# Optimization experiments

Measured on AMD Instinct MI355X. Metric: run time of the kernel, lower is better.

Reference implementation:

```python
import jax, jax.numpy as jnp
import numpy as np

GRID = (32, 32)          # 448 // 14
IMG = (448, 448)
SIGMA = 4.0              # anomalib AnomalyMapGenerator default smoothing


def _l2norm(x, axis=-1, eps=1e-12):
    return x / jnp.clip(jnp.linalg.norm(x, axis=axis, keepdims=True), eps, None)


def _gaussian_blur(x, sigma=SIGMA):
    # kornia-style: kernel_size = 2*int(4*sigma+0.5)+1, reflect padding, separable conv
    radius = int(4.0 * sigma + 0.5)
    t = jnp.arange(-radius, radius + 1, dtype=x.dtype)
    k = jnp.exp(-0.5 * (t / sigma) ** 2)
    k = k / k.sum()
    xp = jnp.pad(x, ((0, 0), (0, 0), (radius, radius), (radius, radius)), mode='reflect')
    kh = k.reshape(1, 1, -1, 1)
    kw = k.reshape(1, 1, 1, -1)
    dn = ('NCHW', 'OIHW', 'NCHW')
    y = jax.lax.conv_general_dilated(xp, kh, (1, 1), 'VALID', dimension_numbers=dn)
    return jax.lax.conv_general_dilated(y, kw, (1, 1), 'VALID', dimension_numbers=dn)


def setup_inputs() -> dict:
    key = jax.random.key(0)
    k1, k2 = jax.random.split(key)
    features = jax.random.normal(k1, (8, 1024, 384), dtype=jnp.float32)
    memory_bank = jax.random.normal(k2, (65536, 384), dtype=jnp.float32)
    return {"features": features, "memory_bank": memory_bank}


def reference(features, memory_bank):
    # features: (B, N, D) patch tokens from DINOv2; memory_bank: (M, D)
    b, n, _ = features.shape
    f = _l2norm(features)                 # F.normalize(features, p=2, dim=1) on flattened patches
    mb = _l2norm(memory_bank)             # bank stores normalized embeddings
    sim = jnp.einsum('bnd,md->bnm', f, mb)            # (B, N, M) cosine similarity
    dists = jnp.clip(1.0 - sim, 0.0, 2.0)
    min_dists = dists.min(axis=2)                     # k = num_neighbours = 1 -> row min
    num_top = max(int(n * 0.01), 1)
    top_vals = jax.lax.top_k(min_dists, num_top)[0]
    pred_score = top_vals.mean(axis=1, keepdims=True) # (B, 1)
    amap = min_dists.reshape(b, 1, *GRID)
    amap = jax.image.resize(amap, (b, 1, *IMG), method='bilinear')
    anomaly_map = _gaussian_blur(amap)                # (B, 1, H, W)
    return pred_score, anomaly_map
```

## Files before the change

### kernel.cpp

```cpp
#include <hip/hip_runtime.h>
#include <hip/hip_bf16.h>

#define NROW_F 8192
#define NROW_B 65536
#define KDIM   384
#define BM 256
#define BN 256
#define NSUB 8
#define NGRP (NROW_B / (BN * NSUB))
#define NBM  (NROW_F / BM)
#define NWG  (NBM * NGRP)

#define LDSA 0
#define LDSB 98304
#define LDSS 147456
#define LDSR 98304
#define LDS_TOT 155648

typedef int   i32x4 __attribute__((ext_vector_type(4)));
typedef float f32x4 __attribute__((ext_vector_type(4)));

static __device__ __forceinline__ void stage16(const void* g, void* l) {
  __builtin_amdgcn_global_load_lds(
      (const __attribute__((address_space(1))) unsigned int*)g,
      (__attribute__((address_space(3))) unsigned int*)l, 16, 0, 0);
}

__global__ __launch_bounds__(256) void quantize_rows_kernel(
    const float* __restrict__ in, char* __restrict__ out8,
    float* __restrict__ scales, int nrows) {
  int row  = blockIdx.x * 4 + (threadIdx.x >> 6);
  int lane = threadIdx.x & 63;
  if (row >= nrows) return;
  const float* r = in + (size_t)row * KDIM;
  float v[6];
  float ss = 0.f, mx = 0.f;
#pragma unroll
  for (int i = 0; i < 6; ++i) {
    v[i] = r[lane + i * 64];
    ss += v[i] * v[i];
    mx = fmaxf(mx, fabsf(v[i]));
  }
#pragma unroll
  for (int d = 1; d < 64; d <<= 1) {
    ss += __shfl_xor(ss, d, 64);
    mx = fmaxf(mx, __shfl_xor(mx, d, 64));
  }
  mx = fmaxf(mx, 1e-30f);
  float inv = rsqrtf(fmaxf(ss, 1e-24f));
  float scl = 127.0f / mx;
  if (lane == 0) scales[row] = mx * inv * (1.0f / 127.0f);
  char* o = out8 + (size_t)row * KDIM;
#pragma unroll
  for (int i = 0; i < 6; ++i)
    o[lane + i * 64] = (char)__float2int_rn(v[i] * scl);
}

__global__ __launch_bounds__(1024) void maxsim_kernel(
    const char* __restrict__ F8,
    const char* __restrict__ B8,
    const float* __restrict__ sA,
    const float* __restrict__ sB,
    float* __restrict__ partial) {
  __shared__ __align__(16) char smem[LDS_TOT];

  const int tid  = threadIdx.x;
  const int wv   = tid >> 6;
  const int lane = tid & 63;
  const int l15  = lane & 15;
  const int lhi  = lane >> 4;
  const int wr   = wv >> 2;
  const int wc   = wv & 3;

  const int wg  = (blockIdx.x & 7) * (NWG / 8) + (blockIdx.x >> 3);
  const int bm  = wg & (NBM - 1);
  const int grp = wg >> 5;
  const size_t brow = (size_t)bm * BM;

  const int srow = tid >> 2;
  const int gsw  = (tid & 3) ^ ((tid >> 3) & 3);

  {
    const char* gA = F8 + (size_t)(brow + srow) * KDIM + gsw * 16;
    char* lA = smem + LDSA + wv * 1024;
#pragma unroll
    for (int kt = 0; kt < 6; ++kt)
      stage16(gA + kt * 64, lA + kt * 16384);
  }
  if (wv < 8)
    stage16((const char*)(sB + (size_t)grp * 2048) + tid * 16,
            smem + LDSS + wv * 1024);

  auto stageB = [&](int s2, int koff, int buf) {
    const char* g = B8 + ((size_t)grp * 2048 + s2 * 256 + srow) * KDIM
                    + koff * 64 + gsw * 16;
    stage16(g, smem + LDSB + buf * 16384 + wv * 1024);
  };
  stageB(0, 0, 0);
  stageB(0, 1, 1);

  const int cof = ((l15 >> 1) & 3) << 4;

  auto ldA8 = [&](int k6, int m) -> i32x4 {
    int byte = k6 * 16384 + (wr * 64 + m * 16 + l15) * 64 + ((lhi << 4) ^ cof);
    return *reinterpret_cast<const i32x4*>(smem + LDSA + byte);
  };
  auto ldB8 = [&](int buf, int n) -> i32x4 {
    int byte = buf * 16384 + (wc * 64 + n * 16 + l15) * 64 + ((lhi << 4) ^ cof);
    return *reinterpret_cast<const i32x4*>(smem + LDSB + byte);
  };

  i32x4 acc[4][4];
  f32x4 vm[4];
#pragma unroll
  for (int m = 0; m < 4; ++m) {
    vm[m] = f32x4{-1e30f, -1e30f, -1e30f, -1e30f};
#pragma unroll
    for (int n = 0; n < 4; ++n) acc[m][n] = i32x4{0, 0, 0, 0};
  }

  asm volatile("s_waitcnt vmcnt(1)" ::: "memory");
  __builtin_amdgcn_s_barrier();

  for (int sub = 0; sub < NSUB; ++sub) {
#pragma unroll
    for (int k6 = 0; k6 < 6; ++k6) {
      i32x4 a[4], b[4];
#pragma unroll
      for (int m = 0; m < 4; ++m) a[m] = ldA8(k6, m);
#pragma unroll
      for (int n = 0; n < 4; ++n) b[n] = ldB8(k6 % 3, n);
      asm volatile("s_waitcnt lgkmcnt(0)" ::: "memory");
      __builtin_amdgcn_sched_barrier(0);
      __builtin_amdgcn_s_setprio(1);
#pragma unroll
      for (int n = 0; n < 4; ++n)
#pragma unroll
        for (int m = 0; m < 4; ++m)
          acc[m][n] = __builtin_amdgcn_mfma_i32_16x16x64_i8(
              a[m], b[n], acc[m][n], 0, 0, 0);
      __builtin_amdgcn_s_setprio(0);
      {
        const int s2   = (k6 < 4) ? sub : ((sub + 1) & 7);
        const int koff = (k6 + 2) % 6;
        stageB(s2, koff, (k6 + 2) % 3);
      }
      asm volatile("s_waitcnt vmcnt(1)" ::: "memory");
      __builtin_amdgcn_s_barrier();
    }
    float sb[4];
#pragma unroll
    for (int n = 0; n < 4; ++n)
      sb[n] = *reinterpret_cast<const float*>(
          smem + LDSS + (sub * 256 + wc * 64 + n * 16 + l15) * 4);
#pragma unroll
    for (int m = 0; m < 4; ++m) {
#pragma unroll
      for (int n = 0; n < 4; ++n)
#pragma unroll
        for (int j = 0; j < 4; ++j)
          vm[m][j] = fmaxf(vm[m][j], (float)acc[m][n][j] * sb[n]);
#pragma unroll
      for (int n = 0; n < 4; ++n) acc[m][n] = i32x4{0, 0, 0, 0};
    }
  }

  asm volatile("s_waitcnt vmcnt(0)" ::: "memory");
#pragma unroll
  for (int d = 1; d < 16; d <<= 1)
#pragma unroll
    for (int m = 0; m < 4; ++m)
#pragma unroll
      for (int j = 0; j < 4; ++j)
        vm[m][j] = fmaxf(vm[m][j], __shfl_xor(vm[m][j], d, 64));

  float* red = (float*)(smem + LDSR);
  __syncthreads();
  if (l15 == 0) {
#pragma unroll
    for (int m = 0; m < 4; ++m)
#pragma unroll
      for (int j = 0; j < 4; ++j)
        red[wc * 256 + wr * 64 + m * 16 + lhi * 4 + j] = vm[m][j];
  }
  __syncthreads();
  if (tid < 256) {
    float x = fmaxf(fmaxf(red[tid], red[256 + tid]),
                    fmaxf(red[512 + tid], red[768 + tid]));
    partial[(size_t)grp * NROW_F + brow + tid] = x * sA[brow + tid];
  }
}

__global__ __launch_bounds__(256) void combine_kernel(
    const float* __restrict__ partial, float* __restrict__ md) {
  int r = blockIdx.x * 256 + threadIdx.x;
  if (r >= NROW_F) return;
  float m = -1e30f;
#pragma unroll
  for (int c = 0; c < NGRP; ++c) m = fmaxf(m, partial[(size_t)c * NROW_F + r]);
  float d = 1.0f - m;
  d = fminf(fmaxf(d, 0.0f), 2.0f);
  md[r] = d;
}

__global__ __launch_bounds__(256) void topk_kernel(
    const float* __restrict__ md, float* __restrict__ out) {
  __shared__ float buf[1024];
  __shared__ float svals[256];
  __shared__ int   sidx[256];
  int b = blockIdx.x, tid = threadIdx.x;
  for (int i = tid; i < 1024; i += 256) buf[i] = md[b * 1024 + i];
  __syncthreads();
  float total = 0.f;
  for (int it = 0; it < 10; ++it) {
    float best = -1e30f; int bi = 0;
    for (int i = tid; i < 1024; i += 256)
      if (buf[i] > best) { best = buf[i]; bi = i; }
    svals[tid] = best; sidx[tid] = bi;
    __syncthreads();
    for (int s = 128; s > 0; s >>= 1) {
      if (tid < s && svals[tid + s] > svals[tid]) {
        svals[tid] = svals[tid + s]; sidx[tid] = sidx[tid + s];
      }
      __syncthreads();
    }
    if (tid == 0) { total += svals[0]; buf[sidx[0]] = -1e30f; }
    __syncthreads();
  }
  if (tid == 0) out[b] = total * 0.1f;
}

__global__ __launch_bounds__(256) void build_w_kernel(float* __restrict__ W) {
  int idx = blockIdx.x * 256 + threadIdx.x;
  if (idx >= 448 * 32) return;
  int y = idx >> 5, g = idx & 31;
  float ksum = 0.f, acc = 0.f;
#pragma unroll
  for (int t = -16; t <= 16; ++t) {
    float ft = (float)t * 0.25f;
    float kv = expf(-0.5f * ft * ft);
    ksum += kv;
    int p = y + t;
    p = (p < 0) ? -p : ((p > 447) ? 894 - p : p);
    float src = ((float)p + 0.5f) * (1.0f / 14.0f) - 0.5f;
    float fl = floorf(src);
    int i0 = (int)fl;
    float fr = src - fl;
    int c0 = i0 < 0 ? 0 : (i0 > 31 ? 31 : i0);
    int i1 = i0 + 1;
    int c1 = i1 < 0 ? 0 : (i1 > 31 ? 31 : i1);
    float w = 0.f;
    if (c0 == g) w += 1.0f - fr;
    if (c1 == g) w += fr;
    acc += kv * w;
  }
  W[idx] = acc / ksum;
}

__global__ __launch_bounds__(256) void map_stage1_kernel(
    const float* __restrict__ md, const float* __restrict__ W,
    float* __restrict__ tmp) {
  int idx = blockIdx.x * 256 + threadIdx.x;
  if (idx >= 8 * 448 * 32) return;
  int gx = idx & 31;
  int y  = (idx >> 5) % 448;
  int b  = idx / (448 * 32);
  const float* w = W + y * 32;
  const float* m = md + b * 1024 + gx;
  float s = 0.f;
#pragma unroll
  for (int gy = 0; gy < 32; ++gy) s += w[gy] * m[gy * 32];
  tmp[idx] = s;
}

__global__ __launch_bounds__(256) void map_stage2_kernel(
    const float* __restrict__ tmp, const float* __restrict__ W,
    float* __restrict__ out) {
  int idx = blockIdx.x * 256 + threadIdx.x;
  if (idx >= 8 * 448 * 448) return;
  int x    = idx % 448;
  int ypos = idx / 448;
  const float* w = W + x * 32;
  const float* t = tmp + ypos * 32;
  float s = 0.f;
#pragma unroll
  for (int gx = 0; gx < 32; ++gx) s += w[gx] * t[gx];
  out[idx] = s;
}

extern "C" void kernel_launch(void* const* d_in, const int* in_sizes, int n_in,
                              void* d_out, int out_size, void* d_ws, size_t ws_size,
                              hipStream_t stream) {
  const float* features = (const float*)d_in[0];
  const float* bank     = (const float*)d_in[1];
  float* out = (float*)d_out;

  char* ws = (char*)d_ws;
  char*  mb8     = ws;
  char*  f8      = ws + 25165824;
  float* sB      = (float*)(ws + 28311552);
  float* sA      = (float*)(ws + 28573696);
  float* partial = (float*)(ws + 28606464);
  float* md      = (float*)(ws + 29655040);
  float* W       = (float*)(ws + 29687808);
  float* tmp     = (float*)(ws + 29745152);

  quantize_rows_kernel<<<NROW_B / 4, 256, 0, stream>>>(bank, mb8, sB, NROW_B);
  quantize_rows_kernel<<<NROW_F / 4, 256, 0, stream>>>(features, f8, sA, NROW_F);
  maxsim_kernel<<<NWG, 1024, 0, stream>>>(f8, mb8, sA, sB, partial);
  combine_kernel<<<NROW_F / 256, 256, 0, stream>>>(partial, md);
  topk_kernel<<<8, 256, 0, stream>>>(md, out);
  build_w_kernel<<<(448 * 32 + 255) / 256, 256, 0, stream>>>(W);
  map_stage1_kernel<<<(8 * 448 * 32 + 255) / 256, 256, 0, stream>>>(md, W, tmp);
  map_stage2_kernel<<<(8 * 448 * 448 + 255) / 256, 256, 0, stream>>>(tmp, W, out + 8);
}
```

Measured before the change: 275.3 us.

## Shrink maxsim workgroup to 256 threads with 128-row tiles and double-buffered B

The maxsim GEMM-max kernel now uses 128-row A tiles and 256-thread workgroups, and each wave computes a 64x128 output tile with 32 accumulators. The LDS footprint drops so two workgroups can share a CU. The B staging moves from triple to double buffering, with a barrier placed before the next prefetch, and the bank scales are read from global memory instead of being staged in LDS. This aims for better occupancy and latency hiding, at the cost of higher register pressure and more workgroups re-reading the bank.

```diff
diff --git a/kernel.cpp b/kernel.cpp
--- a/kernel.cpp
+++ b/kernel.cpp
@@ -4,7 +4,7 @@
 #define NROW_F 8192
 #define NROW_B 65536
 #define KDIM   384
-#define BM 256
+#define BM 128
 #define BN 256
 #define NSUB 8
 #define NGRP (NROW_B / (BN * NSUB))
@@ -12,10 +12,9 @@
 #define NWG  (NBM * NGRP)
 
 #define LDSA 0
-#define LDSB 98304
-#define LDSS 147456
-#define LDSR 98304
-#define LDS_TOT 155648
+#define LDSB 49152
+#define LDSR 49152
+#define LDS_TOT 81920
 
 typedef int   i32x4 __attribute__((ext_vector_type(4)));
 typedef float f32x4 __attribute__((ext_vector_type(4)));
@@ -56,7 +55,7 @@
     o[lane + i * 64] = (char)__float2int_rn(v[i] * scl);
 }
 
-__global__ __launch_bounds__(1024) void maxsim_kernel(
+__global__ __launch_bounds__(256, 2) void maxsim_kernel(
     const char* __restrict__ F8,
     const char* __restrict__ B8,
     const float* __restrict__ sA,
@@ -69,12 +68,12 @@
   const int lane = tid & 63;
   const int l15  = lane & 15;
   const int lhi  = lane >> 4;
-  const int wr   = wv >> 2;
-  const int wc   = wv & 3;
+  const int wr   = wv >> 1;
+  const int wc   = wv & 1;
 
   const int wg  = (blockIdx.x & 7) * (NWG / 8) + (blockIdx.x >> 3);
   const int bm  = wg & (NBM - 1);
-  const int grp = wg >> 5;
+  const int grp = wg >> 6;
   const size_t brow = (size_t)bm * BM;
 
   const int srow = tid >> 2;
@@ -84,17 +83,19 @@
     const char* gA = F8 + (size_t)(brow + srow) * KDIM + gsw * 16;
     char* lA = smem + LDSA + wv * 1024;
 #pragma unroll
-    for (int kt = 0; kt < 6; ++kt)
-      stage16(gA + kt * 64, lA + kt * 16384);
-  }
-  if (wv < 8)
-    stage16((const char*)(sB + (size_t)grp * 2048) + tid * 16,
-            smem + LDSS + wv * 1024);
+    for (int kt = 0; kt < 6; ++kt) {
+      stage16(gA + kt * 64,             lA + kt * 8192);
+      stage16(gA + kt * 64 + 64 * KDIM, lA + kt * 8192 + 4096);
+    }
+  }
 
   auto stageB = [&](int s2, int koff, int buf) {
     const char* g = B8 + ((size_t)grp * 2048 + s2 * 256 + srow) * KDIM
                     + koff * 64 + gsw * 16;
-    stage16(g, smem + LDSB + buf * 16384 + wv * 1024);
+    char* l = smem + LDSB + buf * 16384 + wv * 1024;
+#pragma unroll
+    for (int j = 0; j < 4; ++j)
+      stage16(g + (size_t)(j * 64) * KDIM, l + j * 4096);
   };
   stageB(0, 0, 0);
   stageB(0, 1, 1);
@@ -102,70 +103,72 @@
   const int cof = ((l15 >> 1) & 3) << 4;
 
   auto ldA8 = [&](int k6, int m) -> i32x4 {
-    int byte = k6 * 16384 + (wr * 64 + m * 16 + l15) * 64 + ((lhi << 4) ^ cof);
+    int byte = k6 * 8192 + (wr * 64 + m * 16 + l15) * 64 + ((lhi << 4) ^ cof);
     return *reinterpret_cast<const i32x4*>(smem + LDSA + byte);
   };
   auto ldB8 = [&](int buf, int n) -> i32x4 {
-    int byte = buf * 16384 + (wc * 64 + n * 16 + l15) * 64 + ((lhi << 4) ^ cof);
+    int byte = buf * 16384 + (wc * 128 + n * 16 + l15) * 64 + ((lhi << 4) ^ cof);
     return *reinterpret_cast<const i32x4*>(smem + LDSB + byte);
   };
 
-  i32x4 acc[4][4];
+  i32x4 acc[4][8];
   f32x4 vm[4];
 #pragma unroll
   for (int m = 0; m < 4; ++m) {
     vm[m] = f32x4{-1e30f, -1e30f, -1e30f, -1e30f};
 #pragma unroll
-    for (int n = 0; n < 4; ++n) acc[m][n] = i32x4{0, 0, 0, 0};
-  }
-
-  asm volatile("s_waitcnt vmcnt(1)" ::: "memory");
+    for (int n = 0; n < 8; ++n) acc[m][n] = i32x4{0, 0, 0, 0};
+  }
+
+  asm volatile("s_waitcnt vmcnt(4)" ::: "memory");
   __builtin_amdgcn_s_barrier();
 
   for (int sub = 0; sub < NSUB; ++sub) {
 #pragma unroll
     for (int k6 = 0; k6 < 6; ++k6) {
-      i32x4 a[4], b[4];
+      i32x4 a[4], b[8];
 #pragma unroll
       for (int m = 0; m < 4; ++m) a[m] = ldA8(k6, m);
 #pragma unroll
-      for (int n = 0; n < 4; ++n) b[n] = ldB8(k6 % 3, n);
+      for (int n = 0; n < 8; ++n) b[n] = ldB8(k6 & 1, n);
       asm volatile("s_waitcnt lgkmcnt(0)" ::: "memory");
       __builtin_amdgcn_sched_barrier(0);
+      __builtin_amdgcn_s_barrier();
+
+      {
+        const int s2   = (k6 < 4) ? sub : ((sub + 1) & 7);
+        const int koff = (k6 + 2) % 6;
+        stageB(s2, koff, k6 & 1);
+      }
       __builtin_amdgcn_s_setprio(1);
 #pragma unroll
-      for (int n = 0; n < 4; ++n)
+      for (int n = 0; n < 8; ++n)
 #pragma unroll
         for (int m = 0; m < 4; ++m)
           acc[m][n] = __builtin_amdgcn_mfma_i32_16x16x64_i8(
               a[m], b[n], acc[m][n], 0, 0, 0);
       __builtin_amdgcn_s_setprio(0);
-      {
-        const int s2   = (k6 < 4) ? sub : ((sub + 1) & 7);
-        const int koff = (k6 + 2) % 6;
-        stageB(s2, koff, (k6 + 2) % 3);
-      }
-      asm volatile("s_waitcnt vmcnt(1)" ::: "memory");
+      asm volatile("s_waitcnt vmcnt(4)" ::: "memory");
       __builtin_amdgcn_s_barrier();
     }
-    float sb[4];
-#pragma unroll
-    for (int n = 0; n < 4; ++n)
-      sb[n] = *reinterpret_cast<const float*>(
-          smem + LDSS + (sub * 256 + wc * 64 + n * 16 + l15) * 4);
+    const float* sbp = sB + (size_t)grp * 2048 + sub * 256 + wc * 128 + l15;
+    float sb[8];
+#pragma unroll
+    for (int n = 0; n < 8; ++n) sb[n] = sbp[n * 16];
 #pragma unroll
     for (int m = 0; m < 4; ++m) {
 #pragma unroll
-      for (int n = 0; n < 4; ++n)
+      for (int n = 0; n < 8; ++n)
 #pragma unroll
         for (int j = 0; j < 4; ++j)
           vm[m][j] = fmaxf(vm[m][j], (float)acc[m][n][j] * sb[n]);
 #pragma unroll
-      for (int n = 0; n < 4; ++n) acc[m][n] = i32x4{0, 0, 0, 0};
+      for (int n = 0; n < 8; ++n) acc[m][n] = i32x4{0, 0, 0, 0};
     }
   }
 
   asm volatile("s_waitcnt vmcnt(0)" ::: "memory");
+  __syncthreads();
 #pragma unroll
   for (int d = 1; d < 16; d <<= 1)
 #pragma unroll
@@ -175,18 +178,16 @@
         vm[m][j] = fmaxf(vm[m][j], __shfl_xor(vm[m][j], d, 64));
 
   float* red = (float*)(smem + LDSR);
+  if (l15 == 0) {
+#pragma unroll
+    for (int m = 0; m < 4; ++m)
+#pragma unroll
+      for (int j = 0; j < 4; ++j)
+        red[wc * 128 + wr * 64 + m * 16 + lhi * 4 + j] = vm[m][j];
+  }
   __syncthreads();
-  if (l15 == 0) {
-#pragma unroll
-    for (int m = 0; m < 4; ++m)
-#pragma unroll
-      for (int j = 0; j < 4; ++j)
-        red[wc * 256 + wr * 64 + m * 16 + lhi * 4 + j] = vm[m][j];
-  }
-  __syncthreads();
-  if (tid < 256) {
-    float x = fmaxf(fmaxf(red[tid], red[256 + tid]),
-                    fmaxf(red[512 + tid], red[768 + tid]));
+  if (tid < BM) {
+    float x = fmaxf(red[tid], red[128 + tid]);
     partial[(size_t)grp * NROW_F + brow + tid] = x * sA[brow + tid];
   }
 }
@@ -307,7 +308,7 @@
 
   quantize_rows_kernel<<<NROW_B / 4, 256, 0, stream>>>(bank, mb8, sB, NROW_B);
   quantize_rows_kernel<<<NROW_F / 4, 256, 0, stream>>>(features, f8, sA, NROW_F);
-  maxsim_kernel<<<NWG, 1024, 0, stream>>>(f8, mb8, sA, sB, partial);
+  maxsim_kernel<<<NWG, 256, 0, stream>>>(f8, mb8, sA, sB, partial);
   combine_kernel<<<NROW_F / 256, 256, 0, stream>>>(partial, md);
   topk_kernel<<<8, 256, 0, stream>>>(md, out);
   build_w_kernel<<<(448 * 32 + 255) / 256, 256, 0, stream>>>(W);
```

Measured after the change: 259.4 us. 5.8% less time.
